# Kernel tuning notes

Hardware: AMD Instinct MI355X
Metric: run time of the kernel (lower is better)

Reference implementation:

```python
import jax, jax.numpy as jnp
import numpy as np

N = 100000   # nodes
E = 1600000  # edges (avg degree 16)
D = 64       # in = hidden = out channels
NEG_SLOPE = 0.2
EPS_IN = 1e-5


def setup_inputs() -> dict:
    key = jax.random.key(0)
    ks = jax.random.split(key, 24)
    s = 0.05
    p = lambda k, shape: jax.random.normal(k, shape, jnp.float32) * s
    inp = {
        "x": jax.random.normal(ks[0], (N, D), jnp.float32),
        "edge_index": jax.random.randint(ks[1], (2, E), 0, N, dtype=jnp.int64),
        "edge_attr": jax.random.normal(ks[2], (E, D), jnp.float32),
        # GATv2Conv #1: lin_l, lin_r (bias=True), lin_edge (bias=False), att, out bias
        "Wl1": p(ks[3], (D, D)), "bl1": p(ks[4], (D,)),
        "Wr1": p(ks[5], (D, D)), "br1": p(ks[6], (D,)),
        "We1": p(ks[7], (D, D)), "att1": p(ks[8], (D,)), "bo1": p(ks[9], (D,)),
        # GATv2Conv #2
        "Wl2": p(ks[10], (D, D)), "bl2": p(ks[11], (D,)),
        "Wr2": p(ks[12], (D, D)), "br2": p(ks[13], (D,)),
        "We2": p(ks[14], (D, D)), "att2": p(ks[15], (D,)), "bo2": p(ks[16], (D,)),
        # skip linear
        "Wskip": p(ks[17], (D, D)), "bskip": p(ks[18], (D,)),
    }
    return inp


def _instance_norm(h):
    # InstanceNorm1d on a 2D [N, C] input -> per-row normalization over C, no affine
    mu = h.mean(-1, keepdims=True)
    var = ((h - mu) ** 2).mean(-1, keepdims=True)
    return (h - mu) * jax.lax.rsqrt(var + EPS_IN)


def _gatv2(x, src, dst, edge_attr, Wl, bl, Wr, br, We, att, bo):
    xl = x @ Wl.T + bl          # source-side transform [N, D]
    xr = x @ Wr.T + br          # target-side transform [N, D]
    e = edge_attr @ We.T        # edge transform [E, D]
    m = xl[src] + xr[dst] + e   # per-edge pre-activation [E, D]
    score = jnp.where(m > 0, m, NEG_SLOPE * m) @ att  # [E]
    # segment softmax over edges sharing the same target node
    smax = jax.ops.segment_max(score, dst, num_segments=N)
    smax = jnp.where(jnp.isfinite(smax), smax, 0.0)
    es = jnp.exp(score - smax[dst])
    denom = jax.ops.segment_sum(es, dst, num_segments=N)
    alpha = es / (denom[dst] + 1e-16)  # [E]
    out = jax.ops.segment_sum(alpha[:, None] * xl[src], dst, num_segments=N)
    return out + bo


def reference(x, edge_index, edge_attr,
              Wl1, bl1, Wr1, br1, We1, att1, bo1,
              Wl2, bl2, Wr2, br2, We2, att2, bo2,
              Wskip, bskip):
    src, dst = edge_index[0], edge_index[1]
    h = jax.nn.relu(_gatv2(x, src, dst, edge_attr, Wl1, bl1, Wr1, br1, We1, att1, bo1))
    h = _instance_norm(h)
    h2 = jax.nn.relu(_gatv2(h, src, dst, edge_attr, Wl2, bl2, Wr2, br2, We2, att2, bo2)
                     + x @ Wskip.T + bskip)
    return _instance_norm(h2)
```

## Files before the change

kernel.cpp:

```cpp
#include <hip/hip_runtime.h>

#define DCH 64
#define NEG 0.2f

typedef float fx4 __attribute__((ext_vector_type(4)));
typedef short short8 __attribute__((ext_vector_type(8)));

__device__ __forceinline__ unsigned short f2bf(float f) {
    unsigned int u = __builtin_bit_cast(unsigned int, f);
    u += 0x7fffu + ((u >> 16) & 1u);
    return (unsigned short)(u >> 16);
}
__device__ __forceinline__ float bf2f(unsigned short h) {
    unsigned int u = ((unsigned int)h) << 16;
    return __builtin_bit_cast(float, u);
}

__device__ __forceinline__ short8 pack_bf16x8(fx4 a, fx4 b) {
    short8 r;
    r[0] = (short)f2bf(a[0]); r[1] = (short)f2bf(a[1]);
    r[2] = (short)f2bf(a[2]); r[3] = (short)f2bf(a[3]);
    r[4] = (short)f2bf(b[0]); r[5] = (short)f2bf(b[1]);
    r[6] = (short)f2bf(b[2]); r[7] = (short)f2bf(b[3]);
    return r;
}

__global__ void k_zero(int* __restrict__ p, int n) {
    int i = blockIdx.x * blockDim.x + threadIdx.x;
    if (i < n) p[i] = 0;
}

__global__ void k_count(const int* __restrict__ ei, int* __restrict__ deg, int E) {
    int e = blockIdx.x * blockDim.x + threadIdx.x;
    if (e < E) atomicAdd(&deg[ei[E + e]], 1);
}

__global__ void k_scan1(const int* __restrict__ deg, int* __restrict__ rowptr,
                        int* __restrict__ bsum, int n) {
    __shared__ int s[256];
    int t = threadIdx.x;
    int base = blockIdx.x * 1024 + t * 4;
    int v[4]; int sum = 0;
    #pragma unroll
    for (int j = 0; j < 4; j++) {
        int idx = base + j;
        v[j] = (idx < n) ? deg[idx] : 0;
        sum += v[j];
    }
    s[t] = sum;
    __syncthreads();
    for (int o = 1; o < 256; o <<= 1) {
        int add = (t >= o) ? s[t - o] : 0;
        __syncthreads();
        s[t] += add;
        __syncthreads();
    }
    int excl = s[t] - sum;
    if (t == 255) bsum[blockIdx.x] = s[255];
    int run = excl;
    #pragma unroll
    for (int j = 0; j < 4; j++) {
        int idx = base + j;
        if (idx < n) rowptr[idx] = run;
        run += v[j];
    }
}

__global__ void k_scan2(int* __restrict__ bsum, int nb) {
    int run = 0;
    for (int i = 0; i < nb; i++) { int t = bsum[i]; bsum[i] = run; run += t; }
}

__global__ void k_scan3(int* __restrict__ rowptr, const int* __restrict__ bsum,
                        int n, int E) {
    int i = blockIdx.x * blockDim.x + threadIdx.x;
    if (i < n) rowptr[i] += bsum[i >> 10];
    if (i == 0) rowptr[n] = E;
}

__global__ void k_fill(const int* __restrict__ ei, const int* __restrict__ rowptr,
                       int* __restrict__ cnt, int* __restrict__ csrc,
                       int* __restrict__ iperm, int E) {
    int e = blockIdx.x * blockDim.x + threadIdx.x;
    if (e < E) {
        int t = ei[E + e];
        int p = rowptr[t] + atomicAdd(&cnt[t], 1);
        csrc[p] = ei[e];
        iperm[e] = p;
    }
}

__global__ __launch_bounds__(256) void k_node_gemm(
    const float* __restrict__ X, int nrows,
    const float* __restrict__ Wl, const float* __restrict__ bl, unsigned short* __restrict__ XLB,
    const float* __restrict__ Wr, const float* __restrict__ br, float* __restrict__ XR,
    const float* __restrict__ Wsk, const float* __restrict__ bsk, float* __restrict__ S)
{
    int wid = (blockIdx.x * blockDim.x + threadIdx.x) >> 6;
    int lane = threadIdx.x & 63;
    int ntiles = (nrows + 63) >> 6;
    if (wid >= ntiles) return;
    int base = wid * 64;
    int l15 = lane & 15, q = lane >> 4;

    short8 afr[4][2];
    #pragma unroll
    for (int mt = 0; mt < 4; mt++) {
        int row = base + mt * 16 + l15;
        if (row >= nrows) row = nrows - 1;
        const float* xp = X + (size_t)row * DCH + q * 8;
        #pragma unroll
        for (int kt = 0; kt < 2; kt++) {
            fx4 v0 = *(const fx4*)(xp + kt * 32);
            fx4 v1 = *(const fx4*)(xp + kt * 32 + 4);
            afr[mt][kt] = pack_bf16x8(v0, v1);
        }
    }

    const float* Ws[3] = {Wl, Wr, Wsk};
    const float* bs[3] = {bl, br, bsk};
    int nmat = S ? 3 : 2;

    for (int m = 0; m < nmat; m++) {
        const float* W = Ws[m];
        short8 bfr[4][2];
        #pragma unroll
        for (int nt = 0; nt < 4; nt++) {
            const float* wp = W + (nt * 16 + l15) * DCH + q * 8;
            #pragma unroll
            for (int kt = 0; kt < 2; kt++) {
                fx4 v0 = *(const fx4*)(wp + kt * 32);
                fx4 v1 = *(const fx4*)(wp + kt * 32 + 4);
                bfr[nt][kt] = pack_bf16x8(v0, v1);
            }
        }
        fx4 acc[4][4] = {};
        #pragma unroll
        for (int kt = 0; kt < 2; kt++)
            #pragma unroll
            for (int mt = 0; mt < 4; mt++)
                #pragma unroll
                for (int nt = 0; nt < 4; nt++)
                    acc[mt][nt] = __builtin_amdgcn_mfma_f32_16x16x32_bf16(
                        afr[mt][kt], bfr[nt][kt], acc[mt][nt], 0, 0, 0);

        float bias[4];
        #pragma unroll
        for (int nt = 0; nt < 4; nt++) bias[nt] = bs[m][nt * 16 + l15];
        #pragma unroll
        for (int mt = 0; mt < 4; mt++) {
            #pragma unroll
            for (int r = 0; r < 4; r++) {
                int row = base + mt * 16 + q * 4 + r;
                if (row < nrows) {
                    #pragma unroll
                    for (int nt = 0; nt < 4; nt++) {
                        float v = acc[mt][nt][r] + bias[nt];
                        if (m == 0)
                            XLB[(size_t)row * DCH + nt * 16 + l15] = f2bf(v);
                        else if (m == 1)
                            XR[(size_t)row * DCH + nt * 16 + l15] = v;
                        else
                            S[(size_t)row * DCH + nt * 16 + l15] = v;
                    }
                }
            }
        }
    }
}

__global__ __launch_bounds__(256) void k_edge_tf(
    const float* __restrict__ EA, const int* __restrict__ iperm,
    const float* __restrict__ We1, const float* __restrict__ We2,
    unsigned short* __restrict__ E1, unsigned short* __restrict__ E2, int E)
{
    int wid = (blockIdx.x * blockDim.x + threadIdx.x) >> 6;
    int lane = threadIdx.x & 63;
    int l15 = lane & 15, q = lane >> 4;
    int base = wid * 64;
    if (base >= E) return;

    int p_me = iperm[min(base + lane, E - 1)];

    short8 afr[4][2];
    #pragma unroll
    for (int mt = 0; mt < 4; mt++) {
        int row = min(base + mt * 16 + l15, E - 1);
        const float* p = EA + (size_t)row * DCH + q * 8;
        #pragma unroll
        for (int kt = 0; kt < 2; kt++) {
            fx4 v0 = *(const fx4*)(p + kt * 32);
            fx4 v1 = *(const fx4*)(p + kt * 32 + 4);
            afr[mt][kt] = pack_bf16x8(v0, v1);
        }
    }

    const float* Ws[2] = {We1, We2};
    unsigned short* Es[2] = {E1, E2};
    #pragma unroll
    for (int lyr = 0; lyr < 2; lyr++) {
        const float* W = Ws[lyr];
        short8 bfr[4][2];
        #pragma unroll
        for (int nt = 0; nt < 4; nt++) {
            const float* wp = W + (nt * 16 + l15) * DCH + q * 8;
            #pragma unroll
            for (int kt = 0; kt < 2; kt++) {
                fx4 v0 = *(const fx4*)(wp + kt * 32);
                fx4 v1 = *(const fx4*)(wp + kt * 32 + 4);
                bfr[nt][kt] = pack_bf16x8(v0, v1);
            }
        }
        fx4 acc[4][4] = {};
        #pragma unroll
        for (int kt = 0; kt < 2; kt++)
            #pragma unroll
            for (int mt = 0; mt < 4; mt++)
                #pragma unroll
                for (int nt = 0; nt < 4; nt++)
                    acc[mt][nt] = __builtin_amdgcn_mfma_f32_16x16x32_bf16(
                        afr[mt][kt], bfr[nt][kt], acc[mt][nt], 0, 0, 0);

        unsigned short* Eo = Es[lyr];
        #pragma unroll
        for (int mt = 0; mt < 4; mt++) {
            #pragma unroll
            for (int r = 0; r < 4; r++) {
                int m = mt * 16 + q * 4 + r;
                int pm = __shfl(p_me, m);
                if (base + m < E) {
                    #pragma unroll
                    for (int nt = 0; nt < 4; nt++)
                        Eo[(size_t)pm * DCH + nt * 16 + l15] = f2bf(acc[mt][nt][r]);
                }
            }
        }
    }
}

__global__ __launch_bounds__(256) void k_pull(
    const int* __restrict__ rowptr, const int* __restrict__ csrc,
    const unsigned short* __restrict__ ECSR, const unsigned short* __restrict__ XLB,
    const float* __restrict__ XR, const float* __restrict__ att,
    const float* __restrict__ bo, const float* __restrict__ skip,
    float* __restrict__ out, int n_nodes)
{
    int wid = (blockIdx.x * blockDim.x + threadIdx.x) >> 6;
    int lane = threadIdx.x & 63;
    if (wid >= n_nodes) return;
    int r0 = rowptr[wid], r1 = rowptr[wid + 1];
    float xr_l = XR[(size_t)wid * DCH + lane];
    float att_l = att[lane];
    float acc = 0.f, den = 0.f;

    for (int b = r0; b < r1; b += 64) {
        int cnt = min(64, r1 - b);
        int sj = 0;
        if (lane < cnt) sj = csrc[b + lane];
        int s0 = __shfl(sj, 0);
        unsigned short xl_pf = XLB[(size_t)s0 * DCH + lane];
        unsigned short e_pf = ECSR[(size_t)b * DCH + lane];
        for (int i = 0; i < cnt; i++) {
            float xlv = bf2f(xl_pf);
            float ev = bf2f(e_pf);
            if (i + 1 < cnt) {
                int s1 = __shfl(sj, i + 1);
                xl_pf = XLB[(size_t)s1 * DCH + lane];
                e_pf = ECSR[(size_t)(b + i + 1) * DCH + lane];
            }
            float z = xlv + xr_l + ev;
            float lr = fmaxf(z, 0.f) + NEG * fminf(z, 0.f);
            float t = att_l * lr;
            t += __shfl_xor(t, 1);
            t += __shfl_xor(t, 2);
            t += __shfl_xor(t, 4);
            t += __shfl_xor(t, 8);
            t += __shfl_xor(t, 16);
            t += __shfl_xor(t, 32);
            float w = __expf(t);
            acc = fmaf(w, xlv, acc);
            den += w;
        }
    }

    float v = acc / (den + 1e-16f) + bo[lane];
    if (skip) v += skip[(size_t)wid * DCH + lane];
    v = fmaxf(v, 0.f);
    float mu = v;
    #pragma unroll
    for (int o = 1; o < 64; o <<= 1) mu += __shfl_xor(mu, o);
    mu *= (1.f / 64.f);
    float d = v - mu;
    float var = d * d;
    #pragma unroll
    for (int o = 1; o < 64; o <<= 1) var += __shfl_xor(var, o);
    var *= (1.f / 64.f);
    out[(size_t)wid * DCH + lane] = d * rsqrtf(var + 1e-5f);
}

extern "C" void kernel_launch(void* const* d_in, const int* in_sizes, int n_in,
                              void* d_out, int out_size, void* d_ws, size_t ws_size,
                              hipStream_t stream) {
    const float* x    = (const float*)d_in[0];
    const int*   ei   = (const int*)d_in[1];
    const float* ea   = (const float*)d_in[2];
    const float* Wl1  = (const float*)d_in[3];
    const float* bl1  = (const float*)d_in[4];
    const float* Wr1  = (const float*)d_in[5];
    const float* br1  = (const float*)d_in[6];
    const float* We1  = (const float*)d_in[7];
    const float* att1 = (const float*)d_in[8];
    const float* bo1  = (const float*)d_in[9];
    const float* Wl2  = (const float*)d_in[10];
    const float* bl2  = (const float*)d_in[11];
    const float* Wr2  = (const float*)d_in[12];
    const float* br2  = (const float*)d_in[13];
    const float* We2  = (const float*)d_in[14];
    const float* att2 = (const float*)d_in[15];
    const float* bo2  = (const float*)d_in[16];
    const float* Wsk  = (const float*)d_in[17];
    const float* bsk  = (const float*)d_in[18];
    float* out = (float*)d_out;

    const int N = in_sizes[0] / DCH;
    const int E = in_sizes[1] / 2;

    char* ws = (char*)d_ws;
    size_t off = 0;
    unsigned short* e1  = (unsigned short*)(ws + off); off += (size_t)E * DCH * 2;
    unsigned short* e2  = (unsigned short*)(ws + off); off += (size_t)E * DCH * 2;
    unsigned short* xlb = (unsigned short*)(ws + off); off += (size_t)N * DCH * 2;
    float* xr   = (float*)(ws + off); off += (size_t)N * DCH * 4;
    float* h    = (float*)(ws + off); off += (size_t)N * DCH * 4;
    float* S    = (float*)(ws + off); off += (size_t)N * DCH * 4;
    int* rowptr = (int*)(ws + off);   off += (size_t)(N + 1) * 4;
    int* degcnt = (int*)(ws + off);   off += (size_t)(2 * N) * 4;
    int* csrc   = (int*)(ws + off);   off += (size_t)E * 4;
    int* iperm  = (int*)(ws + off);   off += (size_t)E * 4;
    int* bsum   = (int*)(ws + off);   off += 256 * 4;
    int* deg = degcnt;
    int* cnt = degcnt + N;

    const int nb = (N + 1023) / 1024;

    k_zero<<<(2 * N + 255) / 256, 256, 0, stream>>>(degcnt, 2 * N);
    k_count<<<(E + 255) / 256, 256, 0, stream>>>(ei, deg, E);
    k_scan1<<<nb, 256, 0, stream>>>(deg, rowptr, bsum, N);
    k_scan2<<<1, 1, 0, stream>>>(bsum, nb);
    k_scan3<<<(N + 255) / 256, 256, 0, stream>>>(rowptr, bsum, N, E);
    k_fill<<<(E + 255) / 256, 256, 0, stream>>>(ei, rowptr, cnt, csrc, iperm, E);

    const int node_tiles = (N + 63) / 64;
    const int ng_blocks = (node_tiles + 3) / 4;
    const int eg_blocks = (E / 64 + 3) / 4;
    const int pull_blocks = (N + 3) / 4;

    k_edge_tf<<<eg_blocks, 256, 0, stream>>>(ea, iperm, We1, We2, e1, e2, E);

    k_node_gemm<<<ng_blocks, 256, 0, stream>>>(x, N, Wl1, bl1, xlb, Wr1, br1, xr,
                                               Wsk, bsk, S);
    k_pull<<<pull_blocks, 256, 0, stream>>>(rowptr, csrc, e1, xlb, xr, att1, bo1,
                                            nullptr, h, N);
    k_node_gemm<<<ng_blocks, 256, 0, stream>>>(h, N, Wl2, bl2, xlb, Wr2, br2, xr,
                                               nullptr, nullptr, nullptr);
    k_pull<<<pull_blocks, 256, 0, stream>>>(rowptr, csrc, e2, xlb, xr, att2, bo2,
                                            S, out, N);
}
```

Baseline: 1.299 ms.

## Process four edges per wavefront in pull kernel and vectorize edge-transform stores

The pull kernel now gives each 16-lane group one edge with 4 channels per lane, so a wavefront handles four edges at once. This shortens the cross-lane reduction from six shuffle steps to four and replaces scalar bf16 gathers with 8-byte vector loads. The edge-transform GEMM swaps the operand roles so each lane holds four consecutive channels and can write 8-byte vector stores to the permuted CSR rows. The grid size also rounds up to cover a partial final tile, and the pull kernel drops its software prefetch across iterations.

```diff
diff --git a/kernel.cpp b/kernel.cpp
--- a/kernel.cpp
+++ b/kernel.cpp
@@ -5,6 +5,7 @@
 
 typedef float fx4 __attribute__((ext_vector_type(4)));
 typedef short short8 __attribute__((ext_vector_type(8)));
+typedef unsigned short us4 __attribute__((ext_vector_type(4)));
 
 __device__ __forceinline__ unsigned short f2bf(float f) {
     unsigned int u = __builtin_bit_cast(unsigned int, f);
@@ -182,16 +183,16 @@
 
     int p_me = iperm[min(base + lane, E - 1)];
 
-    short8 afr[4][2];
-    #pragma unroll
-    for (int mt = 0; mt < 4; mt++) {
-        int row = min(base + mt * 16 + l15, E - 1);
+    short8 bfr[4][2];
+    #pragma unroll
+    for (int et = 0; et < 4; et++) {
+        int row = min(base + et * 16 + l15, E - 1);
         const float* p = EA + (size_t)row * DCH + q * 8;
         #pragma unroll
         for (int kt = 0; kt < 2; kt++) {
             fx4 v0 = *(const fx4*)(p + kt * 32);
             fx4 v1 = *(const fx4*)(p + kt * 32 + 4);
-            afr[mt][kt] = pack_bf16x8(v0, v1);
+            bfr[et][kt] = pack_bf16x8(v0, v1);
         }
     }
 
@@ -200,39 +201,41 @@
     #pragma unroll
     for (int lyr = 0; lyr < 2; lyr++) {
         const float* W = Ws[lyr];
-        short8 bfr[4][2];
-        #pragma unroll
-        for (int nt = 0; nt < 4; nt++) {
-            const float* wp = W + (nt * 16 + l15) * DCH + q * 8;
+        short8 afr[4][2];
+        #pragma unroll
+        for (int ct = 0; ct < 4; ct++) {
+            const float* wp = W + (ct * 16 + l15) * DCH + q * 8;
             #pragma unroll
             for (int kt = 0; kt < 2; kt++) {
                 fx4 v0 = *(const fx4*)(wp + kt * 32);
                 fx4 v1 = *(const fx4*)(wp + kt * 32 + 4);
-                bfr[nt][kt] = pack_bf16x8(v0, v1);
+                afr[ct][kt] = pack_bf16x8(v0, v1);
             }
         }
         fx4 acc[4][4] = {};
         #pragma unroll
         for (int kt = 0; kt < 2; kt++)
             #pragma unroll
-            for (int mt = 0; mt < 4; mt++)
+            for (int ct = 0; ct < 4; ct++)
                 #pragma unroll
-                for (int nt = 0; nt < 4; nt++)
-                    acc[mt][nt] = __builtin_amdgcn_mfma_f32_16x16x32_bf16(
-                        afr[mt][kt], bfr[nt][kt], acc[mt][nt], 0, 0, 0);
+                for (int et = 0; et < 4; et++)
+                    acc[ct][et] = __builtin_amdgcn_mfma_f32_16x16x32_bf16(
+                        afr[ct][kt], bfr[et][kt], acc[ct][et], 0, 0, 0);
 
         unsigned short* Eo = Es[lyr];
         #pragma unroll
-        for (int mt = 0; mt < 4; mt++) {
-            #pragma unroll
-            for (int r = 0; r < 4; r++) {
-                int m = mt * 16 + q * 4 + r;
-                int pm = __shfl(p_me, m);
-                if (base + m < E) {
-                    #pragma unroll
-                    for (int nt = 0; nt < 4; nt++)
-                        Eo[(size_t)pm * DCH + nt * 16 + l15] = f2bf(acc[mt][nt][r]);
-                }
+        for (int et = 0; et < 4; et++) {
+            int pm = __shfl(p_me, et * 16 + l15);
+            bool ok = (base + et * 16 + l15) < E;
+            #pragma unroll
+            for (int ct = 0; ct < 4; ct++) {
+                us4 v;
+                v[0] = f2bf(acc[ct][et][0]);
+                v[1] = f2bf(acc[ct][et][1]);
+                v[2] = f2bf(acc[ct][et][2]);
+                v[3] = f2bf(acc[ct][et][3]);
+                if (ok)
+                    *(us4*)(Eo + (size_t)pm * DCH + ct * 16 + q * 4) = v;
             }
         }
     }
@@ -248,54 +251,74 @@
     int wid = (blockIdx.x * blockDim.x + threadIdx.x) >> 6;
     int lane = threadIdx.x & 63;
     if (wid >= n_nodes) return;
+    int g = lane >> 4;
+    int c = lane & 15;
     int r0 = rowptr[wid], r1 = rowptr[wid + 1];
-    float xr_l = XR[(size_t)wid * DCH + lane];
-    float att_l = att[lane];
-    float acc = 0.f, den = 0.f;
-
-    for (int b = r0; b < r1; b += 64) {
-        int cnt = min(64, r1 - b);
-        int sj = 0;
-        if (lane < cnt) sj = csrc[b + lane];
-        int s0 = __shfl(sj, 0);
-        unsigned short xl_pf = XLB[(size_t)s0 * DCH + lane];
-        unsigned short e_pf = ECSR[(size_t)b * DCH + lane];
-        for (int i = 0; i < cnt; i++) {
-            float xlv = bf2f(xl_pf);
-            float ev = bf2f(e_pf);
-            if (i + 1 < cnt) {
-                int s1 = __shfl(sj, i + 1);
-                xl_pf = XLB[(size_t)s1 * DCH + lane];
-                e_pf = ECSR[(size_t)(b + i + 1) * DCH + lane];
-            }
-            float z = xlv + xr_l + ev;
+
+    fx4 xr4 = *(const fx4*)(XR + (size_t)wid * DCH + c * 4);
+    fx4 at4 = *(const fx4*)(att + c * 4);
+    fx4 acc = {0.f, 0.f, 0.f, 0.f};
+    float den = 0.f;
+
+    for (int b = r0; b < r1; b += 4) {
+        int slot = b + g;
+        bool valid = slot < r1;
+        int sl = valid ? slot : (r1 - 1);
+        int src = csrc[sl];
+        us4 xl4 = *(const us4*)(XLB + (size_t)src * DCH + c * 4);
+        us4 e4  = *(const us4*)(ECSR + (size_t)sl * DCH + c * 4);
+        float xv[4]; float p = 0.f;
+        #pragma unroll
+        for (int i = 0; i < 4; i++) {
+            xv[i] = bf2f(xl4[i]);
+            float z = xv[i] + xr4[i] + bf2f(e4[i]);
             float lr = fmaxf(z, 0.f) + NEG * fminf(z, 0.f);
-            float t = att_l * lr;
-            t += __shfl_xor(t, 1);
-            t += __shfl_xor(t, 2);
-            t += __shfl_xor(t, 4);
-            t += __shfl_xor(t, 8);
-            t += __shfl_xor(t, 16);
-            t += __shfl_xor(t, 32);
-            float w = __expf(t);
-            acc = fmaf(w, xlv, acc);
-            den += w;
-        }
-    }
-
-    float v = acc / (den + 1e-16f) + bo[lane];
-    if (skip) v += skip[(size_t)wid * DCH + lane];
-    v = fmaxf(v, 0.f);
-    float mu = v;
-    #pragma unroll
-    for (int o = 1; o < 64; o <<= 1) mu += __shfl_xor(mu, o);
-    mu *= (1.f / 64.f);
-    float d = v - mu;
-    float var = d * d;
-    #pragma unroll
-    for (int o = 1; o < 64; o <<= 1) var += __shfl_xor(var, o);
-    var *= (1.f / 64.f);
-    out[(size_t)wid * DCH + lane] = d * rsqrtf(var + 1e-5f);
+            p = fmaf(at4[i], lr, p);
+        }
+        p += __shfl_xor(p, 1);
+        p += __shfl_xor(p, 2);
+        p += __shfl_xor(p, 4);
+        p += __shfl_xor(p, 8);
+        float w = valid ? __expf(p) : 0.f;
+        #pragma unroll
+        for (int i = 0; i < 4; i++) acc[i] = fmaf(w, xv[i], acc[i]);
+        den += w;
+    }
+
+    #pragma unroll
+    for (int i = 0; i < 4; i++) {
+        acc[i] += __shfl_xor(acc[i], 16);
+        acc[i] += __shfl_xor(acc[i], 32);
+    }
+    den += __shfl_xor(den, 16);
+    den += __shfl_xor(den, 32);
+
+    float inv = 1.f / (den + 1e-16f);
+    float v[4]; float s = 0.f;
+    fx4 sk4 = {0.f, 0.f, 0.f, 0.f};
+    if (skip) sk4 = *(const fx4*)(skip + (size_t)wid * DCH + c * 4);
+    fx4 bo4 = *(const fx4*)(bo + c * 4);
+    #pragma unroll
+    for (int i = 0; i < 4; i++) {
+        v[i] = acc[i] * inv + bo4[i] + sk4[i];
+        v[i] = fmaxf(v[i], 0.f);
+        s += v[i];
+    }
+    s += __shfl_xor(s, 1); s += __shfl_xor(s, 2);
+    s += __shfl_xor(s, 4); s += __shfl_xor(s, 8);
+    float mu = s * (1.f / 64.f);
+    float ss = 0.f;
+    #pragma unroll
+    for (int i = 0; i < 4; i++) { v[i] -= mu; ss += v[i] * v[i]; }
+    ss += __shfl_xor(ss, 1); ss += __shfl_xor(ss, 2);
+    ss += __shfl_xor(ss, 4); ss += __shfl_xor(ss, 8);
+    float rs = rsqrtf(ss * (1.f / 64.f) + 1e-5f);
+    if (g == 0) {
+        fx4 o;
+        #pragma unroll
+        for (int i = 0; i < 4; i++) o[i] = v[i] * rs;
+        *(fx4*)(out + (size_t)wid * DCH + c * 4) = o;
+    }
 }
 
 extern "C" void kernel_launch(void* const* d_in, const int* in_sizes, int n_in,
@@ -352,7 +375,7 @@
 
     const int node_tiles = (N + 63) / 64;
     const int ng_blocks = (node_tiles + 3) / 4;
-    const int eg_blocks = (E / 64 + 3) / 4;
+    const int eg_blocks = ((E + 63) / 64 + 3) / 4;
     const int pull_blocks = (N + 3) / 4;
 
     k_edge_tf<<<eg_blocks, 256, 0, stream>>>(ea, iperm, We1, We2, e1, e2, E);
```

After: 1.201 ms. 7.6% less time.
